# Kernel tuning notes

Measured on AMD Instinct MI355X. Metric: run time of the kernel, lower is better.

Reference implementation:

```python
import jax, jax.numpy as jnp
import numpy as np

T = 32  # simulation_length
L = 4   # number of NeuralCores in the chain


def to_uniform_spikes(x, cycle, sim_len):
    """Uniform spike encoding: emit round(x*T) spikes evenly spaced over T cycles.
    Faithful to SpikingUnifiedCoreFlow.to_uniform_spikes."""
    N = jnp.round(x * sim_len).astype(jnp.int32)
    mask = (N != 0) & (N != sim_len) & (cycle < sim_len)
    N_safe = jnp.maximum(N, 1)
    spacing = sim_len / N_safe.astype(x.dtype)          # T / N
    fire = mask & (jnp.floor(cycle / spacing) < N_safe) & (jnp.floor(jnp.mod(cycle, spacing)) == 0)
    out = fire.astype(x.dtype)
    return jnp.where(N == sim_len, jnp.ones_like(out), out)  # saturated channels fire every cycle


def setup_inputs() -> dict:
    key = jax.random.key(0)
    k0, k1 = jax.random.split(key)
    x = jax.random.uniform(k0, (128, 1024), dtype=jnp.float32)          # activations in [0,1]
    weights = jax.random.normal(k1, (L, 1024, 1024), dtype=jnp.float32) * 0.02  # (neurons, axons) per core
    thresholds = jnp.ones((L,), dtype=jnp.float32)
    return {"x": x, "weights": weights, "thresholds": thresholds}


def reference(x, weights, thresholds):
    """Rate-mode spiking simulation over a chain of NeuralCores.
    Per cycle: encode input to spikes (Uniform), propagate through cores with
    LIF integration (membrane += W @ spikes; spike = threshold < membrane;
    membrane -= spike * threshold), output = mean spike train of last core."""
    B = x.shape[0]
    H = weights.shape[1]

    def step(mem, cycle):
        sig = to_uniform_spikes(x, cycle, T)            # (B, axons_in)
        new_mems = []
        for l in range(L):
            m = mem[l] + sig @ weights[l].T             # F.linear(sig, W)
            s = (thresholds[l] < m).astype(x.dtype)     # thresholding_mode '<'
            m = m - s * thresholds[l]                   # Default firing: subtract reset
            new_mems.append(m)
            sig = s                                     # feed downstream core this cycle
        return jnp.stack(new_mems), sig                 # sig = last core spikes

    mem0 = jnp.zeros((L, B, H), dtype=x.dtype)
    _, out_spikes = jax.lax.scan(step, mem0, jnp.arange(T))  # (T, B, H)
    return out_spikes.mean(axis=0)                      # spike counts -> rates
```

## Files before the change

kernel.cpp:

```cpp
#include <hip/hip_runtime.h>
#include <stdint.h>


typedef __attribute__((ext_vector_type(4)))  int   i32x4;
typedef __attribute__((ext_vector_type(16))) int   i32x16;
typedef __attribute__((ext_vector_type(4)))  float f32x4;

#define SCALE_F 4294967296.0f
#define NSL 4

__device__ __forceinline__ void gload16(const void* g, void* l) {
    __builtin_amdgcn_global_load_lds(
        (const __attribute__((address_space(1))) void*)g,
        (__attribute__((address_space(3))) void*)l, 16, 0, 0);
}

__device__ __forceinline__ i32x4 expand16(unsigned int f) {
    i32x4 r;
    #pragma unroll
    for (int d = 0; d < 4; ++d)
        r[d] = (int)((((f >> (4 * d)) & 0xFu) * 0x00204081u) & 0x01010101u);
    return r;
}

__device__ __forceinline__ void digits4(const float* __restrict__ w,
                                        signed char* __restrict__ planes,
                                        int layer, int rest4) {
    f32x4 wv = *reinterpret_cast<const f32x4*>(w + ((size_t)layer << 20) + rest4);
    long long q[4];
    #pragma unroll
    for (int i = 0; i < 4; ++i) q[i] = llrintf(wv[i] * SCALE_F);
    #pragma unroll
    for (int s = 0; s < NSL; ++s) {
        uint32_t pack = 0;
        #pragma unroll
        for (int i = 0; i < 4; ++i) {
            int d = (int)(signed char)((unsigned char)(q[i] & 255));
            q[i] = (q[i] - d) >> 8;
            pack |= ((uint32_t)(unsigned char)d) << (8 * i);
        }
        *reinterpret_cast<uint32_t*>(planes + (((size_t)(layer * NSL + s)) << 20) + rest4) = pack;
    }
}

__global__ void k_prep(const float* __restrict__ x, const float* __restrict__ w,
                       uint32_t* __restrict__ Am, signed char* __restrict__ planes) {
    if (blockIdx.x < 1024) {
        int tid = blockIdx.x * 256 + threadIdx.x;
        digits4(w, planes, 0, tid << 2);
    } else {
        const int wid  = ((blockIdx.x - 1024) * 256 + threadIdx.x) >> 6;
        const int lane = threadIdx.x & 63;
        const int b = wid >> 4, kc = wid & 15;
        float v = x[b * 1024 + kc * 64 + lane];
        int N = (int)rintf(v * 32.0f);
        uint32_t bits = 0;
        if (N >= 32) {
            bits = 0xFFFFFFFFu;
        } else if (N > 0) {
            float spacing = 32.0f / (float)N;
            #pragma unroll
            for (int t = 0; t < 32; ++t) {
                float fm = fmodf((float)t, spacing);
                if (fm < 1.0f) bits |= (1u << t);
            }
        }
        uint32_t cap = 0;
        #pragma unroll
        for (int t = 0; t < 32; ++t) {
            unsigned long long bal = __ballot((bits >> t) & 1u);
            if (lane == t)      cap = (uint32_t)bal;
            if (lane == t + 32) cap = (uint32_t)(bal >> 32);
        }
        const int t = lane & 31, ww = lane >> 5;
        Am[(size_t)(b * 32 + t) * 32 + kc * 2 + ww] = cap;
    }
}

__global__ __launch_bounds__(512, 4) void k_fused(
        const uint32_t* __restrict__ Am,
        signed char* __restrict__ planes,
        const float* __restrict__ th,
        const float* __restrict__ w,
        uint32_t* __restrict__ AmNext,
        float* __restrict__ out,
        int layer, int dlayer) {
    __shared__ alignas(16) signed char lds[2][32768];

    const int tid  = threadIdx.x;
    const int lane = tid & 63;
    const int wave = tid >> 6;
    const int mw   = wave >> 1;
    const int nw   = wave & 1;
    const int lr   = lane & 31;
    const int hi   = lane >> 5;

    const int xc = blockIdx.x & 7, q = blockIdx.x >> 3;
    const int nTile = xc * 2 + (q & 1);
    const int mTile = q >> 1;
    const int mBase = mTile * 128, nBase = nTile * 64;

    const signed char* srcB[NSL];
    {
        const int r0 = tid >> 3, qs = tid & 7;
        const int sw0 = (qs ^ (r0 & 7)) * 16;
        #pragma unroll
        for (int s = 0; s < NSL; ++s)
            srcB[s] = planes + (((size_t)(layer * NSL + s)) << 20)
                    + (size_t)(nBase + r0) * 1024 + sw0;
    }
    const uint32_t* aRow = Am + (size_t)(mBase + mw * 32 + lr) * 32;

    int baddr[4];
    {
        const int brow = nw * 32 + lr;
        #pragma unroll
        for (int ks = 0; ks < 4; ++ks)
            baddr[ks] = brow * 128 + (((ks * 2 + hi) ^ (brow & 7)) * 16);
    }

    i32x16 acc[NSL];
    #pragma unroll
    for (int s = 0; s < NSL; ++s)
        #pragma unroll
        for (int r = 0; r < 16; ++r) acc[s][r] = 0;

    auto H0 = [&](int buf, int c) {
        const int ko = c * 128;
        gload16(srcB[0] + ko, &lds[buf][0]    + tid * 16);
        gload16(srcB[1] + ko, &lds[buf][8192] + tid * 16);
    };
    auto H1 = [&](int buf, int c) {
        const int ko = c * 128;
        gload16(srcB[2] + ko, &lds[buf][16384] + tid * 16);
        gload16(srcB[3] + ko, &lds[buf][24576] + tid * 16);
    };

    i32x4 amr[2];
    H0(0, 0);
    amr[0] = *reinterpret_cast<const i32x4*>(aRow);
    H1(0, 0);

    #pragma unroll
    for (int c = 0; c < 8; ++c) {
        const int buf = c & 1;
        const signed char* lb = &lds[buf][0];

        asm volatile("s_waitcnt vmcnt(2)" ::: "memory");
        __builtin_amdgcn_s_barrier();
        asm volatile("" ::: "memory");

        if (c + 1 < 8) {
            H0(buf ^ 1, c + 1);
            amr[(c + 1) & 1] = *reinterpret_cast<const i32x4*>(aRow + (c + 1) * 4);
            H1(buf ^ 1, c + 1);
        }

        i32x4 af[4];
        __builtin_amdgcn_s_setprio(1);
        #pragma unroll
        for (int ks = 0; ks < 4; ++ks) {
            af[ks] = expand16((((unsigned)amr[c & 1][ks]) >> (16 * hi)) & 0xFFFFu);
            #pragma unroll
            for (int s = 0; s < 2; ++s) {
                i32x4 bf = *reinterpret_cast<const i32x4*>(lb + s * 8192 + baddr[ks]);
                acc[s] = __builtin_amdgcn_mfma_i32_32x32x32_i8(af[ks], bf, acc[s], 0, 0, 0);
            }
        }
        __builtin_amdgcn_s_setprio(0);

        if (c + 1 < 8) asm volatile("s_waitcnt vmcnt(5)" ::: "memory");
        else           asm volatile("s_waitcnt vmcnt(0)" ::: "memory");
        __builtin_amdgcn_s_barrier();
        asm volatile("" ::: "memory");

        __builtin_amdgcn_s_setprio(1);
        #pragma unroll
        for (int ks = 0; ks < 4; ++ks) {
            #pragma unroll
            for (int s = 0; s < 2; ++s) {
                i32x4 bf = *reinterpret_cast<const i32x4*>(lb + (2 + s) * 8192 + baddr[ks]);
                acc[2 + s] = __builtin_amdgcn_mfma_i32_32x32x32_i8(af[ks], bf, acc[2 + s], 0, 0, 0);
            }
        }
        __builtin_amdgcn_s_setprio(0);
    }

    const long long TH = llrintf(th[layer] * SCALE_F);
    const int batch = mTile * 4 + mw;
    uint32_t bits = 0;
    long long mmem = 0;
    #pragma unroll
    for (int half = 0; half < 2; ++half) {
        long long own[8], par[8];
        #pragma unroll
        for (int r = 0; r < 8; ++r) {
            long long v = 0;
            #pragma unroll
            for (int s = 0; s < NSL; ++s)
                v += ((long long)acc[s][half * 8 + r]) << (8 * s);
            own[r] = v;
        }
        #pragma unroll
        for (int r = 0; r < 8; ++r) {
            int plo = __shfl((int)(uint32_t)own[r], lane ^ 32, 64);
            int phi = __shfl((int)(own[r] >> 32), lane ^ 32, 64);
            par[r] = ((long long)phi << 32) | (uint32_t)plo;
        }
        #pragma unroll
        for (int tq = 0; tq < 16; ++tq) {
            const int idx = (tq >> 3) * 4 + (tq & 3);
            const int usePar = ((tq >> 2) & 1) ^ hi;
            long long v = usePar ? par[idx] : own[idx];
            mmem += v;
            if (mmem > TH) { mmem -= TH; bits |= (1u << (half * 16 + tq)); }
        }
    }

    if (AmNext) {
        uint32_t cap = 0;
        #pragma unroll
        for (int t = 0; t < 32; ++t) {
            unsigned long long bal = __ballot((bits >> t) & 1u);
            if (lane == t) cap = (uint32_t)bal;
        }
        if (hi == 0)
            AmNext[(size_t)(batch * 32 + lr) * 32 + nTile * 2 + nw] = cap;
    } else if (hi == 0) {
        out[batch * 1024 + nBase + nw * 32 + lr] = (float)__popc(bits) * 0.03125f;
    }

    if (dlayer < 4)
        digits4(w, planes, dlayer, (blockIdx.x * 512 + tid) << 2);
}

extern "C" void kernel_launch(void* const* d_in, const int* in_sizes, int n_in,
                              void* d_out, int out_size, void* d_ws, size_t ws_size,
                              hipStream_t stream) {
    const float* x  = (const float*)d_in[0];
    const float* w  = (const float*)d_in[1];
    const float* th = (const float*)d_in[2];
    float* out = (float*)d_out;
    char* ws = (char*)d_ws;

    signed char* planes = (signed char*)(ws);
    uint32_t*    Am0    = (uint32_t*)(ws + 16777216);
    uint32_t*    Am1    = (uint32_t*)(ws + 17301504);

    k_prep<<<1536, 256, 0, stream>>>(x, w, Am0, planes);

    uint32_t* Ain = Am0;
    uint32_t* Anx = Am1;
    for (int l = 0; l < 4; ++l) {
        k_fused<<<512, 512, 0, stream>>>(Ain, planes, th, w,
                                         (l < 3) ? Anx : nullptr,
                                         (l == 3) ? out : nullptr,
                                         l, l + 1);
        uint32_t* tmp = Ain; Ain = Anx; Anx = tmp;
    }
}
```

Measured before the change: 102.8 us.

## Store weight digit planes in k-group-major layout for contiguous LDS staging

Changes the layout of the int8 weight digit planes from row-major (row*1024+k) to k-group-major blocks of 16 bytes per row (g*16384 + row*16). The GEMM kernel's B-tile loads then read contiguous 1 KB runs per k-group instead of strided row segments, and LDS addressing drops the XOR swizzle. The prep kernel now processes four quads per thread with fewer blocks. The unswizzled LDS layout risks bank conflicts on the MFMA operand reads, and the weight reads during quantization become more strided.

```diff
diff --git a/kernel.cpp b/kernel.cpp
--- a/kernel.cpp
+++ b/kernel.cpp
@@ -23,33 +23,38 @@
     return r;
 }
 
-__device__ __forceinline__ void digits4(const float* __restrict__ w,
-                                        signed char* __restrict__ planes,
-                                        int layer, int rest4) {
-    f32x4 wv = *reinterpret_cast<const f32x4*>(w + ((size_t)layer << 20) + rest4);
-    long long q[4];
-    #pragma unroll
-    for (int i = 0; i < 4; ++i) q[i] = llrintf(wv[i] * SCALE_F);
+__device__ __forceinline__ void digits_q(const float* __restrict__ w,
+                                         signed char* __restrict__ planes,
+                                         int layer, int unit, int q) {
+    const int row = unit & 1023, g = unit >> 10;
+    f32x4 wv = *reinterpret_cast<const f32x4*>(
+            w + ((size_t)layer << 20) + (size_t)row * 1024 + g * 16 + q * 4);
+    long long qq[4];
+    #pragma unroll
+    for (int i = 0; i < 4; ++i) qq[i] = llrintf(wv[i] * SCALE_F);
     #pragma unroll
     for (int s = 0; s < NSL; ++s) {
         uint32_t pack = 0;
         #pragma unroll
         for (int i = 0; i < 4; ++i) {
-            int d = (int)(signed char)((unsigned char)(q[i] & 255));
-            q[i] = (q[i] - d) >> 8;
+            int d = (int)(signed char)((unsigned char)(qq[i] & 255));
+            qq[i] = (qq[i] - d) >> 8;
             pack |= ((uint32_t)(unsigned char)d) << (8 * i);
         }
-        *reinterpret_cast<uint32_t*>(planes + (((size_t)(layer * NSL + s)) << 20) + rest4) = pack;
+        *reinterpret_cast<uint32_t*>(planes + (((size_t)(layer * NSL + s)) << 20)
+                                     + (size_t)g * 16384 + row * 16 + q * 4) = pack;
     }
 }
 
 __global__ void k_prep(const float* __restrict__ x, const float* __restrict__ w,
                        uint32_t* __restrict__ Am, signed char* __restrict__ planes) {
-    if (blockIdx.x < 1024) {
-        int tid = blockIdx.x * 256 + threadIdx.x;
-        digits4(w, planes, 0, tid << 2);
+    if (blockIdx.x < 256) {
+        int unit = blockIdx.x * 256 + threadIdx.x;
+        #pragma unroll
+        for (int q = 0; q < 4; ++q)
+            digits_q(w, planes, 0, unit, q);
     } else {
-        const int wid  = ((blockIdx.x - 1024) * 256 + threadIdx.x) >> 6;
+        const int wid  = ((blockIdx.x - 256) * 256 + threadIdx.x) >> 6;
         const int lane = threadIdx.x & 63;
         const int b = wid >> 4, kc = wid & 15;
         float v = x[b * 1024 + kc * 64 + lane];
@@ -102,12 +107,12 @@
 
     const signed char* srcB[NSL];
     {
-        const int r0 = tid >> 3, qs = tid & 7;
-        const int sw0 = (qs ^ (r0 & 7)) * 16;
+        const int ks0 = tid >> 6;
+        const int rr  = tid & 63;
         #pragma unroll
         for (int s = 0; s < NSL; ++s)
             srcB[s] = planes + (((size_t)(layer * NSL + s)) << 20)
-                    + (size_t)(nBase + r0) * 1024 + sw0;
+                    + (size_t)ks0 * 16384 + (size_t)(nBase + rr) * 16;
     }
     const uint32_t* aRow = Am + (size_t)(mBase + mw * 32 + lr) * 32;
 
@@ -116,7 +121,7 @@
         const int brow = nw * 32 + lr;
         #pragma unroll
         for (int ks = 0; ks < 4; ++ks)
-            baddr[ks] = brow * 128 + (((ks * 2 + hi) ^ (brow & 7)) * 16);
+            baddr[ks] = (ks * 2 + hi) * 1024 + brow * 16;
     }
 
     i32x16 acc[NSL];
@@ -126,12 +131,12 @@
         for (int r = 0; r < 16; ++r) acc[s][r] = 0;
 
     auto H0 = [&](int buf, int c) {
-        const int ko = c * 128;
+        const int ko = c * 131072;
         gload16(srcB[0] + ko, &lds[buf][0]    + tid * 16);
         gload16(srcB[1] + ko, &lds[buf][8192] + tid * 16);
     };
     auto H1 = [&](int buf, int c) {
-        const int ko = c * 128;
+        const int ko = c * 131072;
         gload16(srcB[2] + ko, &lds[buf][16384] + tid * 16);
         gload16(srcB[3] + ko, &lds[buf][24576] + tid * 16);
     };
@@ -230,8 +235,10 @@
         out[batch * 1024 + nBase + nw * 32 + lr] = (float)__popc(bits) * 0.03125f;
     }
 
-    if (dlayer < 4)
-        digits4(w, planes, dlayer, (blockIdx.x * 512 + tid) << 2);
+    if (dlayer < 4) {
+        const int gtid = blockIdx.x * 512 + tid;
+        digits_q(w, planes, dlayer, gtid >> 2, gtid & 3);
+    }
 }
 
 extern "C" void kernel_launch(void* const* d_in, const int* in_sizes, int n_in,
@@ -247,7 +254,7 @@
     uint32_t*    Am0    = (uint32_t*)(ws + 16777216);
     uint32_t*    Am1    = (uint32_t*)(ws + 17301504);
 
-    k_prep<<<1536, 256, 0, stream>>>(x, w, Am0, planes);
+    k_prep<<<768, 256, 0, stream>>>(x, w, Am0, planes);
 
     uint32_t* Ain = Am0;
     uint32_t* Anx = Am1;
```

New measurement: 105.2 us. 1.02x slower.
